# Kernel tuning notes

Measured on AMD Instinct MI355X. Metric: run time of the kernel, lower is better.

The kernel has to match this reference:

```python
import jax, jax.numpy as jnp
import numpy as np
import math

NN_K = 32          # num_neighbor = ceil(k/dilation) = 32
MAP_SIZE = 32
GROUP = 4


def _fibonacci_sphere(samples):
    # matches fibonacci_sphere(samples, randomize=False): rnd = 1.0
    pts = [[0.0, 0.0, 0.0]]
    offset = 2.0 / samples
    increment = math.pi * (3.0 - math.sqrt(5.0))
    for i in range(samples - 1):
        y = i * offset - 1 + offset / 2.0
        r = math.sqrt(1.0 - y * y)
        phi = ((i + 1.0) % samples) * increment
        pts.append([math.cos(phi) * r, y, math.sin(phi) * r])
    return np.asarray(pts, dtype=np.float32)


def setup_inputs() -> dict:
    B, N, C_in, C_out = 8, 2048, 64, 128
    key = jax.random.key(0)
    ks = jax.random.split(key, 6)
    x = jax.random.normal(ks[0], (B, 3, N), dtype=jnp.float32)
    feature = jax.random.normal(ks[1], (B, C_in, N), dtype=jnp.float32)
    neigh_indexs = jax.random.randint(ks[2], (B, N, NN_K), 0, N, dtype=jnp.int32)
    B_rff = jax.random.normal(ks[3], (7, MAP_SIZE), dtype=jnp.float32)  # frozen RFF proj
    kernels = jnp.asarray(_fibonacci_sphere(NN_K).T)                    # [3, NN_K], frozen
    mlp_w = jax.random.normal(ks[4], (C_in, 2 * MAP_SIZE), dtype=jnp.float32) * 0.05
    mlp_b = jnp.zeros((C_in,), dtype=jnp.float32)
    conv_w = jax.random.normal(ks[5], (C_out, 2 * C_in * NN_K), dtype=jnp.float32) * 0.02
    conv_b = jnp.zeros((C_out,), dtype=jnp.float32)
    return {"x": x, "feature": feature, "neigh_indexs": neigh_indexs,
            "B_rff": B_rff, "kernels": kernels,
            "mlp_w": mlp_w, "mlp_b": mlp_b, "conv_w": conv_w, "conv_b": conv_b}


def _topkmax(perm):
    # two normalization passes over axis=1 (rows), squaring in between, then hard threshold
    perm = perm / (jnp.sum(perm, axis=1, keepdims=True) + 1e-6)
    perm = perm * perm
    perm = perm / (jnp.sum(perm, axis=1, keepdims=True) + 1e-6)
    return jnp.where(perm > 0.1, perm, 0.0)


def _paiconv(x, feature, neigh_indexs, B_rff, kernels, mlp_w, mlp_b, conv_w, conv_b):
    bsz, C, N = feature.shape           # B, num_feat, num_pts
    nn_k = neigh_indexs.shape[-1]
    xp = jnp.transpose(x, (0, 2, 1))    # [B, N, 3]

    # neighbor gather of coordinates -> [B*N, nn, 3]
    x_neighs = jax.vmap(lambda p, i: p[i])(xp, neigh_indexs).reshape(bsz * N, nn_k, 3)
    x_rep = jnp.broadcast_to(x_neighs[:, :1, :], x_neighs.shape)
    x_rel = x_neighs - x_rep
    x_dis = jnp.linalg.norm(x_rel, axis=-1, keepdims=True)

    # random Fourier features + 1x1 conv (mlp)
    pos = (2.0 * math.pi) * jnp.concatenate([x_rep, x_rel, x_dis], axis=-1)  # [BN, nn, 7]
    xf = pos @ B_rff                                                          # [BN, nn, 32]
    xf = jnp.concatenate([jnp.sin(xf), jnp.cos(xf)], axis=-1)                 # [BN, nn, 64]
    xf = jnp.einsum('oc,bnc->bon', mlp_w, xf) + mlp_b[None, :, None]          # [BN, C, nn]

    # neighbor gather of features -> [BN, C, nn], concat with positional feats
    fp = jnp.transpose(feature, (0, 2, 1))                                    # [B, N, C]
    f_nb = jax.vmap(lambda p, i: p[i])(fp, neigh_indexs).reshape(bsz * N, nn_k, C)
    feats = jnp.concatenate([jnp.transpose(f_nb, (0, 2, 1)), xf], axis=1)     # [BN, 2C, nn]

    # permutation/attention matrix
    one_pad = jnp.zeros((nn_k, nn_k), dtype=x.dtype).at[0, 0].set(1.0)
    perm = x_rel @ kernels + one_pad                                          # [BN, nn, nn]
    perm = jnp.where(perm > 0, perm, 0.0)
    perm = _topkmax(perm)

    if C > 3:  # static channel shuffle with group=4
        feats = feats.reshape(bsz * N, GROUP, 2 * C // GROUP, nn_k)
        feats = jnp.transpose(feats, (0, 2, 1, 3)).reshape(bsz * N, 2 * C, nn_k)

    feats = feats @ perm                                                      # [BN, 2C, nn]
    feats = feats.reshape(bsz * N, 2 * C * nn_k)
    out = feats @ conv_w.T + conv_b                                           # [BN, out_c]
    return jnp.transpose(out.reshape(bsz, N, -1), (0, 2, 1))                  # [B, out_c, N]


def reference(x, feature, neigh_indexs, B_rff, kernels, mlp_w, mlp_b, conv_w, conv_b):
    return _paiconv(x, feature, neigh_indexs, B_rff, kernels, mlp_w, mlp_b, conv_w, conv_b)
```

## Files before the change

### kernel.cpp

```cpp
#include <hip/hip_runtime.h>

typedef unsigned short ushort_t;
typedef __attribute__((ext_vector_type(8))) short short8;
typedef __attribute__((ext_vector_type(4))) float floatx4;

#define TWO_PI 6.28318530717958647692f

__device__ __forceinline__ float bf2f(ushort_t u) {
  union { unsigned u; float f; } v; v.u = ((unsigned)u) << 16; return v.f;
}
__device__ __forceinline__ ushort_t f2bf(float f) {
  union { float f; unsigned u; } v; v.f = f;
  unsigned r = v.u + 0x7FFFu + ((v.u >> 16) & 1u);
  return (ushort_t)(r >> 16);
}
__device__ __forceinline__ unsigned pk(float a, float b) {
  return (unsigned)f2bf(a) | ((unsigned)f2bf(b) << 16);
}
__device__ __forceinline__ float ldin(const void* p, int idx, bool bf) {
  return bf ? bf2f(((const ushort_t*)p)[idx]) : ((const float*)p)[idx];
}
__device__ __forceinline__ bool detect_bf16(const void* xv) {
  const ushort_t* us = (const ushort_t*)xv;
  unsigned u = us[threadIdx.x & 63];
  int e = (u >> 7) & 0xFF;
  bool good = (e >= 110) && (e <= 133);
  unsigned long long m = __ballot(good);
  return __builtin_popcountll(m) >= 52;
}
__device__ __forceinline__ uint4 pack8f(const float* p) {
  float4 a = *(const float4*)p, b = *(const float4*)(p + 4);
  uint4 r;
  r.x = pk(a.x, a.y); r.y = pk(a.z, a.w);
  r.z = pk(b.x, b.y); r.w = pk(b.z, b.w);
  return r;
}

__global__ __launch_bounds__(256) void paiconv_prep(
    const void* __restrict__ xprobe, const void* __restrict__ feat,
    ushort_t* __restrict__ Ft, const void* __restrict__ W,
    ushort_t* __restrict__ Wc)
{
  const bool bfm = detect_bf16(xprobe);
  const int t = threadIdx.x;
  __shared__ ushort_t tile[64 * 72];

  if (blockIdx.x >= 256) {
    int i = ((blockIdx.x - 256) * 256 + t) << 3;
    if (bfm) *(uint4*)(Wc + i) = *(const uint4*)((const ushort_t*)W + i);
    else     *(uint4*)(Wc + i) = pack8f((const float*)W + i);
    return;
  }

  const int bb = blockIdx.x >> 5;
  const int n0 = (blockIdx.x & 31) << 6;
  {
    const int c = t & 63, ng = t >> 6;
    size_t base = (((size_t)(bb * 64 + c)) << 11) + n0 + (ng << 4);
    ushort_t v[16];
    if (bfm) {
      const ushort_t* fp_ = (const ushort_t*)feat + base;
      uint4 a = *(const uint4*)fp_, b2 = *(const uint4*)(fp_ + 8);
      unsigned uu[8] = {a.x, a.y, a.z, a.w, b2.x, b2.y, b2.z, b2.w};
#pragma unroll
      for (int e = 0; e < 8; ++e) {
        v[2 * e] = (ushort_t)(uu[e] & 0xffff);
        v[2 * e + 1] = (ushort_t)(uu[e] >> 16);
      }
    } else {
      const float* fp_ = (const float*)feat + base;
#pragma unroll
      for (int k = 0; k < 16; ++k) v[k] = f2bf(fp_[k]);
    }
#pragma unroll
    for (int k = 0; k < 16; ++k) tile[(ng * 16 + k) * 72 + c] = v[k];
  }
  __syncthreads();
  {
    const int nn = t >> 2, qtr = t & 3;
    uint4 w0 = *(const uint4*)(tile + nn * 72 + qtr * 16);
    uint4 w1 = *(const uint4*)(tile + nn * 72 + qtr * 16 + 8);
    ushort_t* dst = Ft + (((size_t)(bb * 2048 + n0 + nn)) << 6) + (qtr << 4);
    *(uint4*)dst = w0;
    *(uint4*)(dst + 8) = w1;
  }
}

__global__ __launch_bounds__(256) void paiconv_phase1(
    const void* __restrict__ x,
    const ushort_t* __restrict__ Ft,
    const int*  __restrict__ nbr,
    const void* __restrict__ Brff,
    const void* __restrict__ kern,
    const void* __restrict__ mlpw,
    const void* __restrict__ mlpb,
    ushort_t*   __restrict__ Ag)
{
  const bool bfm = detect_bf16(x);
  const int t = threadIdx.x;
  const int p0 = blockIdx.x << 1;
  const int b  = p0 >> 11;
  const int w = t >> 6, lane = t & 63, lrow = lane & 15, quad = lane >> 4;

  __shared__ ushort_t sRt[64 * 72];
  __shared__ ushort_t sF[2 * 128 * 40];
  __shared__ ushort_t sP[2 * 32 * 40];
  __shared__ float sRel[2][32][3];
  __shared__ float sDis[2][32];
  __shared__ float sRep[2][3];
  __shared__ float sBr[224];
  __shared__ float sKn[96];
  __shared__ float sMb[64];

  const int gpt = t >> 7, gj = (t >> 2) & 31, gch = t & 3;
  const int gidx = nbr[((p0 + gpt) << 5) + gj];
  const ushort_t* gfr = Ft + (((size_t)(b * 2048 + gidx)) << 6) + (gch << 4);
  uint4 g0 = ((const uint4*)gfr)[0];
  uint4 g1 = ((const uint4*)gfr)[1];

  const int mc = (w << 4) + lrow;
  short8 mb0, mb1;
  if (bfm) {
    const ushort_t* mp = (const ushort_t*)mlpw + mc * 64;
    mb0 = *(const short8*)(mp + (quad << 3));
    mb1 = *(const short8*)(mp + 32 + (quad << 3));
  } else {
    const float* mp = (const float*)mlpw + mc * 64;
    uint4 u0 = pack8f(mp + (quad << 3));
    uint4 u1 = pack8f(mp + 32 + (quad << 3));
    mb0 = *(short8*)&u0;
    mb1 = *(short8*)&u1;
  }

  if (t < 224) sBr[t] = ldin(Brff, t, bfm);
  if (t < 96)  sKn[t] = ldin(kern, t, bfm);
  if (t < 64)  sMb[t] = ldin(mlpb, t, bfm);
  if (t < 64) {
    int pt = t >> 5, i = t & 31;
    int p = p0 + pt;
    int idx  = nbr[(p << 5) + i];
    int idx0 = nbr[(p << 5)];
    int xo = b * 6144;
    float rx = ldin(x, xo + idx0, bfm);
    float ry = ldin(x, xo + 2048 + idx0, bfm);
    float rz = ldin(x, xo + 4096 + idx0, bfm);
    float cx = ldin(x, xo + idx, bfm);
    float cy = ldin(x, xo + 2048 + idx, bfm);
    float cz = ldin(x, xo + 4096 + idx, bfm);
    float dx = cx - rx, dy = cy - ry, dz = cz - rz;
    sRel[pt][i][0] = dx; sRel[pt][i][1] = dy; sRel[pt][i][2] = dz;
    sDis[pt][i] = sqrtf(dx * dx + dy * dy + dz * dz);
    if (i == 0) { sRep[pt][0] = rx; sRep[pt][1] = ry; sRep[pt][2] = rz; }
  }
  __syncthreads();

  {
    int jn = t >> 2, mh = (t & 3) << 3;
    int pt = jn >> 5, j = jn & 31;
    float pos[7];
    pos[0] = TWO_PI * sRep[pt][0]; pos[1] = TWO_PI * sRep[pt][1];
    pos[2] = TWO_PI * sRep[pt][2];
    pos[3] = TWO_PI * sRel[pt][j][0]; pos[4] = TWO_PI * sRel[pt][j][1];
    pos[5] = TWO_PI * sRel[pt][j][2];
    pos[6] = TWO_PI * sDis[pt][j];
    unsigned sw[4], cw[4];
#pragma unroll
    for (int mm = 0; mm < 8; mm += 2) {
      float a0 = 0.f, a1 = 0.f;
#pragma unroll
      for (int d = 0; d < 7; ++d) {
        a0 += pos[d] * sBr[d * 32 + mh + mm];
        a1 += pos[d] * sBr[d * 32 + mh + mm + 1];
      }
      sw[mm >> 1] = pk(__sinf(a0), __sinf(a1));
      cw[mm >> 1] = pk(__cosf(a0), __cosf(a1));
    }
    ushort_t* rb = sRt + jn * 72;
    *(uint4*)(rb + mh)      = make_uint4(sw[0], sw[1], sw[2], sw[3]);
    *(uint4*)(rb + 32 + mh) = make_uint4(cw[0], cw[1], cw[2], cw[3]);
  }

  if (t < 64) {
    int pt = t >> 5, j = t & 31;
    float k0 = sKn[j], k1 = sKn[32 + j], k2 = sKn[64 + j];
    float col[32];
    float s1 = 0.f;
#pragma unroll
    for (int i = 0; i < 32; ++i) {
      float v = sRel[pt][i][0] * k0 + sRel[pt][i][1] * k1 + sRel[pt][i][2] * k2;
      if (i == 0 && j == 0) v += 1.0f;
      v = fmaxf(v, 0.f);
      col[i] = v; s1 += v;
    }
    float inv1 = 1.0f / (s1 + 1e-6f);
    float s2 = 0.f;
#pragma unroll
    for (int i = 0; i < 32; ++i) { float v = col[i] * inv1; v = v * v; col[i] = v; s2 += v; }
    float inv2 = 1.0f / (s2 + 1e-6f);
    unsigned pw[16];
#pragma unroll
    for (int i = 0; i < 32; i += 2) {
      float v0 = col[i] * inv2;     v0 = (v0 > 0.1f) ? v0 : 0.f;
      float v1 = col[i + 1] * inv2; v1 = (v1 > 0.1f) ? v1 : 0.f;
      pw[i >> 1] = pk(v0, v1);
    }
    ushort_t* dst = sP + pt * 1280 + j * 40;
#pragma unroll
    for (int g = 0; g < 4; ++g)
      *(uint4*)(dst + g * 8) = make_uint4(pw[4 * g], pw[4 * g + 1], pw[4 * g + 2], pw[4 * g + 3]);
  }
  __syncthreads();

  {
    int row = (mc & 31) * 4 + 2 + (mc >> 5);
    float bv = sMb[mc];
#pragma unroll
    for (int mt = 0; mt < 4; ++mt) {
      const ushort_t* rp = sRt + (mt * 16 + lrow) * 72 + (quad << 3);
      short8 a0 = *(const short8*)rp;
      short8 a1 = *(const short8*)(rp + 32);
      floatx4 acc = {0.f, 0.f, 0.f, 0.f};
      acc = __builtin_amdgcn_mfma_f32_16x16x32_bf16(a0, mb0, acc, 0, 0, 0);
      acc = __builtin_amdgcn_mfma_f32_16x16x32_bf16(a1, mb1, acc, 0, 0, 0);
      int pt = mt >> 1;
      int j0 = ((mt & 1) << 4) + (quad << 2);
      *(uint2*)(sF + pt * 5120 + row * 40 + j0) =
          make_uint2(pk(acc[0] + bv, acc[1] + bv), pk(acc[2] + bv, acc[3] + bv));
    }
  }
  {
    ushort_t* fp_ = sF + gpt * 5120 + (gch >> 1) * 40 + (gch & 1) * 2560 + gj;
    unsigned uu[8] = {g0.x, g0.y, g0.z, g0.w, g1.x, g1.y, g1.z, g1.w};
#pragma unroll
    for (int u = 0; u < 8; ++u) {
      fp_[(2 * u) * 160]     = (ushort_t)(uu[u] & 0xffff);
      fp_[(2 * u + 1) * 160] = (ushort_t)(uu[u] >> 16);
    }
  }
  __syncthreads();

  {
#pragma unroll
    for (int pt = 0; pt < 2; ++pt) {
      const ushort_t* Pp = sP + pt * 1280;
      short8 a0 = *(const short8*)(Pp + lrow * 40 + (quad << 3));
      short8 a1 = *(const short8*)(Pp + (16 + lrow) * 40 + (quad << 3));
      size_t prow = ((size_t)(p0 + pt)) << 12;
#pragma unroll
      for (int nt = 0; nt < 2; ++nt) {
        int cidx = ((w * 2 + nt) << 4) + lrow;
        short8 bfg = *(const short8*)(sF + pt * 5120 + cidx * 40 + (quad << 3));
        floatx4 z = {0.f, 0.f, 0.f, 0.f};
        floatx4 c0 = __builtin_amdgcn_mfma_f32_16x16x32_bf16(a0, bfg, z, 0, 0, 0);
        floatx4 c1 = __builtin_amdgcn_mfma_f32_16x16x32_bf16(a1, bfg, z, 0, 0, 0);
        ushort_t* ad = Ag + prow + cidx * 32 + (quad << 2);
        *(uint2*)ad        = make_uint2(pk(c0[0], c0[1]), pk(c0[2], c0[3]));
        *(uint2*)(ad + 16) = make_uint2(pk(c1[0], c1[1]), pk(c1[2], c1[3]));
      }
    }
  }
}

__global__ __launch_bounds__(256) void paiconv_gemm(
    const ushort_t* __restrict__ A,
    const ushort_t* __restrict__ Wc,
    float* __restrict__ part)
{
  __shared__ ushort_t lA[2][64 * 72];
  __shared__ ushort_t lB[2][128 * 72];
  const int m0 = blockIdx.x << 6;
  const int K0 = blockIdx.y << 11;
  const int t = threadIdx.x;
  const int w = t >> 6, lane = t & 63;
  const int wm = w & 1, wn = w >> 1, lrow = lane & 15, quad = lane >> 4;

  const int ar = t >> 2, ac = (t & 3) << 4;
  const int wr = t >> 1, wc = (t & 1) << 5;
  const ushort_t* Ap = A + (size_t)(m0 + ar) * 4096 + K0 + ac;
  const ushort_t* Wp = Wc + (size_t)wr * 4096 + K0 + wc;

  uint4 ra0 = *(const uint4*)Ap, ra1 = *(const uint4*)(Ap + 8);
  uint4 rb0 = *(const uint4*)Wp, rb1 = *(const uint4*)(Wp + 8);
  uint4 rb2 = *(const uint4*)(Wp + 16), rb3 = *(const uint4*)(Wp + 24);

  floatx4 acc[2][4];
#pragma unroll
  for (int i = 0; i < 2; ++i)
#pragma unroll
    for (int j = 0; j < 4; ++j) acc[i][j] = (floatx4){0.f, 0.f, 0.f, 0.f};

  for (int kb = 0; kb < 32; ++kb) {
    uint4 na0, na1, nb0, nb1, nb2, nb3;
    if (kb < 31) {
      int off = (kb + 1) << 6;
      na0 = *(const uint4*)(Ap + off);      na1 = *(const uint4*)(Ap + off + 8);
      nb0 = *(const uint4*)(Wp + off);      nb1 = *(const uint4*)(Wp + off + 8);
      nb2 = *(const uint4*)(Wp + off + 16); nb3 = *(const uint4*)(Wp + off + 24);
    }
    ushort_t* la = lA[kb & 1];
    ushort_t* lb = lB[kb & 1];
    *(uint4*)(la + ar * 72 + ac)      = ra0;
    *(uint4*)(la + ar * 72 + ac + 8)  = ra1;
    *(uint4*)(lb + wr * 72 + wc)      = rb0;
    *(uint4*)(lb + wr * 72 + wc + 8)  = rb1;
    *(uint4*)(lb + wr * 72 + wc + 16) = rb2;
    *(uint4*)(lb + wr * 72 + wc + 24) = rb3;
    __syncthreads();

#pragma unroll
    for (int kk = 0; kk < 2; ++kk) {
      short8 af0 = *(const short8*)(la + ((wm << 5) + lrow) * 72 + (kk << 5) + (quad << 3));
      short8 af1 = *(const short8*)(la + ((wm << 5) + 16 + lrow) * 72 + (kk << 5) + (quad << 3));
#pragma unroll
      for (int ni = 0; ni < 4; ++ni) {
        short8 bf = *(const short8*)(lb + ((wn << 6) + (ni << 4) + lrow) * 72 +
                                     (kk << 5) + (quad << 3));
        acc[0][ni] = __builtin_amdgcn_mfma_f32_16x16x32_bf16(af0, bf, acc[0][ni], 0, 0, 0);
        acc[1][ni] = __builtin_amdgcn_mfma_f32_16x16x32_bf16(af1, bf, acc[1][ni], 0, 0, 0);
      }
    }
    ra0 = na0; ra1 = na1;
    rb0 = nb0; rb1 = nb1; rb2 = nb2; rb3 = nb3;
  }

  float* dst = part + ((size_t)blockIdx.y << 21);
#pragma unroll
  for (int mi = 0; mi < 2; ++mi)
#pragma unroll
    for (int ni = 0; ni < 4; ++ni)
#pragma unroll
      for (int r = 0; r < 4; ++r) {
        int m = m0 + (wm << 5) + (mi << 4) + (quad << 2) + r;
        int n = (wn << 6) + (ni << 4) + lrow;
        dst[(size_t)m * 128 + n] = acc[mi][ni][r];
      }
}

__global__ __launch_bounds__(256) void paiconv_reduce(
    const void* __restrict__ xprobe, const float* __restrict__ part,
    const void* __restrict__ bias, void* __restrict__ out)
{
  const bool bfm = detect_bf16(xprobe);
  __shared__ float buf[128 * 65];
  const int m0 = blockIdx.x << 6;
  const int b = m0 >> 11, n0 = m0 & 2047;
  const int t = threadIdx.x;

#pragma unroll 4
  for (int i = 0; i < 32; ++i) {
    int idx = i * 256 + t;
    int mt = idx >> 7, c = idx & 127;
    size_t o = (size_t)(m0 + mt) * 128 + c;
    float s = ldin(bias, c, bfm) + part[o] + part[(1u << 21) + o];
    buf[c * 65 + mt] = s;
  }
  __syncthreads();
#pragma unroll 4
  for (int i = 0; i < 32; ++i) {
    int idx = i * 256 + t;
    int c = idx >> 6, nl = idx & 63;
    float v = buf[c * 65 + nl];
    size_t o = (size_t)b * 262144 + (size_t)c * 2048 + n0 + nl;
    if (bfm) ((ushort_t*)out)[o] = f2bf(v);
    else     ((float*)out)[o] = v;
  }
}

extern "C" void kernel_launch(void* const* d_in, const int* in_sizes, int n_in,
                              void* d_out, int out_size, void* d_ws, size_t ws_size,
                              hipStream_t stream) {
  const void* x     = d_in[0];
  const void* feat  = d_in[1];
  const int*  nbr   = (const int*)d_in[2];
  const void* Brff  = d_in[3];
  const void* kern  = d_in[4];
  const void* mlpw  = d_in[5];
  const void* mlpb  = d_in[6];
  const void* convw = d_in[7];
  const void* convb = d_in[8];

  char* ws = (char*)d_ws;
  ushort_t* A   = (ushort_t*)ws;
  ushort_t* Wcv = (ushort_t*)(ws + (size_t)134217728);
  float*    prt = (float*)(ws + (size_t)135266304);
  ushort_t* Ft  = (ushort_t*)(ws + (size_t)152043520);

  paiconv_prep<<<512, 256, 0, stream>>>(x, feat, Ft, convw, Wcv);
  paiconv_phase1<<<8192, 256, 0, stream>>>(x, Ft, nbr, Brff, kern, mlpw, mlpb, A);
  paiconv_gemm<<<dim3(256, 2, 1), 256, 0, stream>>>(A, Wcv, prt);
  paiconv_reduce<<<256, 256, 0, stream>>>(x, prt, convb, d_out);
}
```

Measured before the change: 182.1 us.

## Unshuffle channel layout via weight permutation, halve GEMM M-tile, vectorize reduce

The channel shuffle is moved out of phase1's scattered LDS row mapping and into a permutation of the conv weight columns during prep. Phase1 now writes features in natural channel order with a per-block padded LDS layout (SFPT stride) meant to reduce bank conflicts. The GEMM tile shrinks from 64 to 32 rows with single-buffered LDS, doubling the grid for more occupancy and parallelism at the cost of losing the register prefetch overlap. The reduce kernel switches to float4 loads and 4-wide stores.

```diff
diff --git a/kernel.cpp b/kernel.cpp
--- a/kernel.cpp
+++ b/kernel.cpp
@@ -47,8 +47,11 @@
 
   if (blockIdx.x >= 256) {
     int i = ((blockIdx.x - 256) * 256 + t) << 3;
-    if (bfm) *(uint4*)(Wc + i) = *(const uint4*)((const ushort_t*)W + i);
-    else     *(uint4*)(Wc + i) = pack8f((const float*)W + i);
+    int n = i >> 12, rem = i & 4095;
+    int c = rem >> 5, j = rem & 31;
+    int src = (n << 12) + (((c & 31) * 4 + (c >> 5)) << 5) + j;
+    if (bfm) *(uint4*)(Wc + i) = *(const uint4*)((const ushort_t*)W + src);
+    else     *(uint4*)(Wc + i) = pack8f((const float*)W + src);
     return;
   }
 
@@ -86,6 +89,7 @@
   }
 }
 
+#define SFPT 5184
 __global__ __launch_bounds__(256) void paiconv_phase1(
     const void* __restrict__ x,
     const ushort_t* __restrict__ Ft,
@@ -103,7 +107,7 @@
   const int w = t >> 6, lane = t & 63, lrow = lane & 15, quad = lane >> 4;
 
   __shared__ ushort_t sRt[64 * 72];
-  __shared__ ushort_t sF[2 * 128 * 40];
+  __shared__ ushort_t sF[2 * SFPT];
   __shared__ ushort_t sP[2 * 32 * 40];
   __shared__ float sRel[2][32][3];
   __shared__ float sDis[2][32];
@@ -212,7 +216,8 @@
   __syncthreads();
 
   {
-    int row = (mc & 31) * 4 + 2 + (mc >> 5);
+    int row = 64 + mc;
+    int rbase = row * 40 + ((4 + w) << 3);
     float bv = sMb[mc];
 #pragma unroll
     for (int mt = 0; mt < 4; ++mt) {
@@ -224,17 +229,17 @@
       acc = __builtin_amdgcn_mfma_f32_16x16x32_bf16(a1, mb1, acc, 0, 0, 0);
       int pt = mt >> 1;
       int j0 = ((mt & 1) << 4) + (quad << 2);
-      *(uint2*)(sF + pt * 5120 + row * 40 + j0) =
+      *(uint2*)(sF + pt * SFPT + rbase + j0) =
           make_uint2(pk(acc[0] + bv, acc[1] + bv), pk(acc[2] + bv, acc[3] + bv));
     }
   }
   {
-    ushort_t* fp_ = sF + gpt * 5120 + (gch >> 1) * 40 + (gch & 1) * 2560 + gj;
+    ushort_t* fp_ = sF + gpt * SFPT + gch * 648 + gj;
     unsigned uu[8] = {g0.x, g0.y, g0.z, g0.w, g1.x, g1.y, g1.z, g1.w};
 #pragma unroll
     for (int u = 0; u < 8; ++u) {
-      fp_[(2 * u) * 160]     = (ushort_t)(uu[u] & 0xffff);
-      fp_[(2 * u + 1) * 160] = (ushort_t)(uu[u] >> 16);
+      fp_[(2 * u) * 40]     = (ushort_t)(uu[u] & 0xffff);
+      fp_[(2 * u + 1) * 40] = (ushort_t)(uu[u] >> 16);
     }
   }
   __syncthreads();
@@ -248,8 +253,9 @@
       size_t prow = ((size_t)(p0 + pt)) << 12;
 #pragma unroll
       for (int nt = 0; nt < 2; ++nt) {
-        int cidx = ((w * 2 + nt) << 4) + lrow;
-        short8 bfg = *(const short8*)(sF + pt * 5120 + cidx * 40 + (quad << 3));
+        int blk = w * 2 + nt;
+        int cidx = (blk << 4) + lrow;
+        short8 bfg = *(const short8*)(sF + pt * SFPT + cidx * 40 + (blk << 3) + (quad << 3));
         floatx4 z = {0.f, 0.f, 0.f, 0.f};
         floatx4 c0 = __builtin_amdgcn_mfma_f32_16x16x32_bf16(a0, bfg, z, 0, 0, 0);
         floatx4 c1 = __builtin_amdgcn_mfma_f32_16x16x32_bf16(a1, bfg, z, 0, 0, 0);
@@ -266,72 +272,65 @@
     const ushort_t* __restrict__ Wc,
     float* __restrict__ part)
 {
-  __shared__ ushort_t lA[2][64 * 72];
-  __shared__ ushort_t lB[2][128 * 72];
-  const int m0 = blockIdx.x << 6;
+  __shared__ ushort_t lA[32 * 72];
+  __shared__ ushort_t lB[128 * 72];
+  const int m0 = blockIdx.x << 5;
   const int K0 = blockIdx.y << 11;
   const int t = threadIdx.x;
-  const int w = t >> 6, lane = t & 63;
-  const int wm = w & 1, wn = w >> 1, lrow = lane & 15, quad = lane >> 4;
-
-  const int ar = t >> 2, ac = (t & 3) << 4;
-  const int wr = t >> 1, wc = (t & 1) << 5;
-  const ushort_t* Ap = A + (size_t)(m0 + ar) * 4096 + K0 + ac;
-  const ushort_t* Wp = Wc + (size_t)wr * 4096 + K0 + wc;
-
-  uint4 ra0 = *(const uint4*)Ap, ra1 = *(const uint4*)(Ap + 8);
+  const int w = t >> 6, lane = t & 63, lrow = lane & 15, quad = lane >> 4;
+
+  const int ar = t >> 3, acl = (t & 7) << 3;
+  const int wr = t >> 1, wcl = (t & 1) << 5;
+  const ushort_t* Ap = A + (size_t)(m0 + ar) * 4096 + K0 + acl;
+  const ushort_t* Wp = Wc + (size_t)wr * 4096 + K0 + wcl;
+
+  uint4 ra  = *(const uint4*)Ap;
   uint4 rb0 = *(const uint4*)Wp, rb1 = *(const uint4*)(Wp + 8);
   uint4 rb2 = *(const uint4*)(Wp + 16), rb3 = *(const uint4*)(Wp + 24);
 
-  floatx4 acc[2][4];
+  floatx4 acc[2][2];
 #pragma unroll
   for (int i = 0; i < 2; ++i)
 #pragma unroll
-    for (int j = 0; j < 4; ++j) acc[i][j] = (floatx4){0.f, 0.f, 0.f, 0.f};
+    for (int j = 0; j < 2; ++j) acc[i][j] = (floatx4){0.f, 0.f, 0.f, 0.f};
 
   for (int kb = 0; kb < 32; ++kb) {
-    uint4 na0, na1, nb0, nb1, nb2, nb3;
+    *(uint4*)(lA + ar * 72 + acl)      = ra;
+    *(uint4*)(lB + wr * 72 + wcl)      = rb0;
+    *(uint4*)(lB + wr * 72 + wcl + 8)  = rb1;
+    *(uint4*)(lB + wr * 72 + wcl + 16) = rb2;
+    *(uint4*)(lB + wr * 72 + wcl + 24) = rb3;
+    __syncthreads();
     if (kb < 31) {
       int off = (kb + 1) << 6;
-      na0 = *(const uint4*)(Ap + off);      na1 = *(const uint4*)(Ap + off + 8);
-      nb0 = *(const uint4*)(Wp + off);      nb1 = *(const uint4*)(Wp + off + 8);
-      nb2 = *(const uint4*)(Wp + off + 16); nb3 = *(const uint4*)(Wp + off + 24);
-    }
-    ushort_t* la = lA[kb & 1];
-    ushort_t* lb = lB[kb & 1];
-    *(uint4*)(la + ar * 72 + ac)      = ra0;
-    *(uint4*)(la + ar * 72 + ac + 8)  = ra1;
-    *(uint4*)(lb + wr * 72 + wc)      = rb0;
-    *(uint4*)(lb + wr * 72 + wc + 8)  = rb1;
-    *(uint4*)(lb + wr * 72 + wc + 16) = rb2;
-    *(uint4*)(lb + wr * 72 + wc + 24) = rb3;
-    __syncthreads();
-
+      ra  = *(const uint4*)(Ap + off);
+      rb0 = *(const uint4*)(Wp + off);      rb1 = *(const uint4*)(Wp + off + 8);
+      rb2 = *(const uint4*)(Wp + off + 16); rb3 = *(const uint4*)(Wp + off + 24);
+    }
 #pragma unroll
     for (int kk = 0; kk < 2; ++kk) {
-      short8 af0 = *(const short8*)(la + ((wm << 5) + lrow) * 72 + (kk << 5) + (quad << 3));
-      short8 af1 = *(const short8*)(la + ((wm << 5) + 16 + lrow) * 72 + (kk << 5) + (quad << 3));
-#pragma unroll
-      for (int ni = 0; ni < 4; ++ni) {
-        short8 bf = *(const short8*)(lb + ((wn << 6) + (ni << 4) + lrow) * 72 +
+      short8 af0 = *(const short8*)(lA + lrow * 72 + (kk << 5) + (quad << 3));
+      short8 af1 = *(const short8*)(lA + (16 + lrow) * 72 + (kk << 5) + (quad << 3));
+#pragma unroll
+      for (int ni = 0; ni < 2; ++ni) {
+        short8 bf = *(const short8*)(lB + ((w << 5) + (ni << 4) + lrow) * 72 +
                                      (kk << 5) + (quad << 3));
         acc[0][ni] = __builtin_amdgcn_mfma_f32_16x16x32_bf16(af0, bf, acc[0][ni], 0, 0, 0);
         acc[1][ni] = __builtin_amdgcn_mfma_f32_16x16x32_bf16(af1, bf, acc[1][ni], 0, 0, 0);
       }
     }
-    ra0 = na0; ra1 = na1;
-    rb0 = nb0; rb1 = nb1; rb2 = nb2; rb3 = nb3;
+    __syncthreads();
   }
 
   float* dst = part + ((size_t)blockIdx.y << 21);
 #pragma unroll
   for (int mi = 0; mi < 2; ++mi)
 #pragma unroll
-    for (int ni = 0; ni < 4; ++ni)
+    for (int ni = 0; ni < 2; ++ni)
 #pragma unroll
       for (int r = 0; r < 4; ++r) {
-        int m = m0 + (wm << 5) + (mi << 4) + (quad << 2) + r;
-        int n = (wn << 6) + (ni << 4) + lrow;
+        int m = m0 + (mi << 4) + (quad << 2) + r;
+        int n = (w << 5) + (ni << 4) + lrow;
         dst[(size_t)m * 128 + n] = acc[mi][ni][r];
       }
 }
@@ -346,23 +345,28 @@
   const int b = m0 >> 11, n0 = m0 & 2047;
   const int t = threadIdx.x;
 
-#pragma unroll 4
-  for (int i = 0; i < 32; ++i) {
-    int idx = i * 256 + t;
+#pragma unroll
+  for (int i = 0; i < 8; ++i) {
+    int idx = (i * 256 + t) << 2;
     int mt = idx >> 7, c = idx & 127;
     size_t o = (size_t)(m0 + mt) * 128 + c;
-    float s = ldin(bias, c, bfm) + part[o] + part[(1u << 21) + o];
-    buf[c * 65 + mt] = s;
-  }
-  __syncthreads();
-#pragma unroll 4
-  for (int i = 0; i < 32; ++i) {
-    int idx = i * 256 + t;
+    float4 v0 = *(const float4*)(part + o);
+    float4 v1 = *(const float4*)(part + (1u << 21) + o);
+    buf[(c + 0) * 65 + mt] = v0.x + v1.x + ldin(bias, c + 0, bfm);
+    buf[(c + 1) * 65 + mt] = v0.y + v1.y + ldin(bias, c + 1, bfm);
+    buf[(c + 2) * 65 + mt] = v0.z + v1.z + ldin(bias, c + 2, bfm);
+    buf[(c + 3) * 65 + mt] = v0.w + v1.w + ldin(bias, c + 3, bfm);
+  }
+  __syncthreads();
+#pragma unroll
+  for (int i = 0; i < 8; ++i) {
+    int idx = (i * 256 + t) << 2;
     int c = idx >> 6, nl = idx & 63;
-    float v = buf[c * 65 + nl];
+    float v0 = buf[c * 65 + nl], v1 = buf[c * 65 + nl + 1];
+    float v2 = buf[c * 65 + nl + 2], v3 = buf[c * 65 + nl + 3];
     size_t o = (size_t)b * 262144 + (size_t)c * 2048 + n0 + nl;
-    if (bfm) ((ushort_t*)out)[o] = f2bf(v);
-    else     ((float*)out)[o] = v;
+    if (bfm) *(uint2*)((ushort_t*)out + o) = make_uint2(pk(v0, v1), pk(v2, v3));
+    else     *(float4*)((float*)out + o) = make_float4(v0, v1, v2, v3);
   }
 }
 
@@ -387,6 +391,6 @@
 
   paiconv_prep<<<512, 256, 0, stream>>>(x, feat, Ft, convw, Wcv);
   paiconv_phase1<<<8192, 256, 0, stream>>>(x, Ft, nbr, Brff, kern, mlpw, mlpb, A);
-  paiconv_gemm<<<dim3(256, 2, 1), 256, 0, stream>>>(A, Wcv, prt);
+  paiconv_gemm<<<dim3(512, 2, 1), 256, 0, stream>>>(A, Wcv, prt);
   paiconv_reduce<<<256, 256, 0, stream>>>(x, prt, convb, d_out);
 }
```

Measured after the change: 192.5 us. 5.7% more time.
